# Optimization experiments

Hardware: AMD Instinct MI355X
Metric: run time of the kernel (lower is better)

## Reference

```python
import jax, jax.numpy as jnp
import numpy as np

NUM_HEADS = 16
HEAD_DIM = 64  # latent_dim // num_heads = 1024 // 16


def setup_inputs() -> dict:
    key = jax.random.key(0)
    k1, k2, k3, k4 = jax.random.split(key, 4)
    B, S, C = 4, 2048, 1024
    x = jax.random.normal(k1, (B, S, C), dtype=jnp.float32)
    # torch nn.Linear weight layout: [out_features, in_features]
    W_qkv = jax.random.normal(k2, (2 * 1024 + C, C), dtype=jnp.float32) * (C ** -0.5)
    W_out = jax.random.normal(k3, (C, C), dtype=jnp.float32) * (C ** -0.5)
    b_out = jax.random.normal(k4, (C,), dtype=jnp.float32) * 0.01
    return {"x": x, "W_qkv": W_qkv, "W_out": W_out, "b_out": b_out}


def reference(x, W_qkv, W_out, b_out):
    B, S, C = x.shape
    H, CH = NUM_HEADS, HEAD_DIM
    qkv = jnp.einsum('bsc,oc->bso', x, W_qkv)          # [B, S, 2*latent + C]
    qkv = qkv.reshape(B, S, H, -1)                      # per-head: [CH, CH, C//H]
    q = qkv[..., :CH]
    k = qkv[..., CH:2 * CH]
    v = qkv[..., 2 * CH:]
    energy = jnp.einsum('bqhc,bkhc->bhqk', q, k)        # full score matrix
    scale = jnp.asarray(C, x.dtype) ** 0.5              # note: original scales by sqrt(C), not sqrt(head_dim)
    attn = jax.nn.softmax(energy / scale, axis=-1)
    out = jnp.einsum('bhqk,bkhc->bqhc', attn, v).reshape(B, S, -1)
    out = jnp.einsum('bsc,oc->bso', out, W_out) + b_out
    return out + x
```

## Files before the change

kernel.cpp:

```cpp
#include <hip/hip_runtime.h>
#include <hip/hip_bf16.h>
#include <stdint.h>

#define BB 4
#define SS 2048
#define CC 1024
#define HH 16
#define DD 64
#define MTOT (BB*SS)
#define NQKV 3072

typedef __attribute__((ext_vector_type(8))) short short8;
typedef __attribute__((ext_vector_type(4))) float f32x4;

#define MFMA16(A,B,C) __builtin_amdgcn_mfma_f32_16x16x32_bf16((A),(B),(C),0,0,0)

__device__ __forceinline__ ushort f2bf(float f) {
  uint32_t u = __builtin_bit_cast(uint32_t, f);
  u += 0x7FFFu + ((u >> 16) & 1u);
  return (ushort)(u >> 16);
}

__device__ __forceinline__ unsigned cvtpk(float lo, float hi) {
  unsigned r;
  asm("v_cvt_pk_bf16_f32 %0, %1, %2" : "=v"(r) : "v"(lo), "v"(hi));
  return r;
}

__device__ __forceinline__ float hw_exp2(float x) {
  float r;
  asm("v_exp_f32 %0, %1" : "=v"(r) : "v"(x));
  return r;
}

__global__ void cvt_kernel(const float* __restrict__ src, ushort* __restrict__ dst, int n4) {
  int stride = gridDim.x * blockDim.x;
  for (int i = blockIdx.x * blockDim.x + threadIdx.x; i < n4; i += stride) {
    float4 v = reinterpret_cast<const float4*>(src)[i];
    ushort4 o;
    o.x = f2bf(v.x); o.y = f2bf(v.y); o.z = f2bf(v.z); o.w = f2bf(v.w);
    reinterpret_cast<ushort4*>(dst)[i] = o;
  }
}

__device__ __forceinline__ void stage8k(const ushort* g0, int ldk, ushort* lds, int wave, int lane) {
  #pragma unroll
  for (int r = 0; r < 2; ++r) {
    int chunk = r * 256 + wave * 64 + lane;
    int row = chunk >> 2;
    int co  = (chunk & 3) * 8;
    const ushort* src = g0 + (size_t)row * ldk + co;
    ushort* dst = lds + (size_t)(r * 256 + wave * 64) * 8;
    __builtin_amdgcn_global_load_lds(
        (const __attribute__((address_space(1))) uint32_t*)src,
        (__attribute__((address_space(3))) uint32_t*)dst, 16, 0, 0);
  }
}

__device__ __forceinline__ void gemm_loop(const ushort* __restrict__ A, const ushort* __restrict__ Bw,
                                          int m0, int n0, ushort* As, ushort* Bs, f32x4 acc[4][4]) {
  const int lane = threadIdx.x & 63, wave = threadIdx.x >> 6;
  const int g = lane >> 4, q = lane & 15;
  const int wm = (wave >> 1) * 64, wn = (wave & 1) * 64;
  const ushort* Ag = A + (size_t)m0 * 1024;
  const ushort* Bg = Bw + (size_t)n0 * 1024;
  #pragma unroll 1
  for (int k0 = 0; k0 < 1024; k0 += 32) {
    stage8k(Ag + k0, 1024, As, wave, lane);
    stage8k(Bg + k0, 1024, Bs, wave, lane);
    __syncthreads();
    short8 af[4], bf[4];
    #pragma unroll
    for (int i = 0; i < 4; ++i)
      af[i] = *(const short8*)(As + (wm + i * 16 + q) * 32 + g * 8);
    #pragma unroll
    for (int j = 0; j < 4; ++j)
      bf[j] = *(const short8*)(Bs + (wn + j * 16 + q) * 32 + g * 8);
    #pragma unroll
    for (int i = 0; i < 4; ++i)
      #pragma unroll
      for (int j = 0; j < 4; ++j)
        acc[i][j] = MFMA16(af[i], bf[j], acc[i][j]);
    __syncthreads();
  }
}

__global__ __launch_bounds__(256) void gemm_qkv(const ushort* __restrict__ xb, const ushort* __restrict__ wqkv,
                                                ushort* __restrict__ qfbuf, ushort* __restrict__ kfbuf,
                                                ushort* __restrict__ vfbuf) {
  __shared__ ushort As[128 * 32], Bs[128 * 32];
  const int m0 = blockIdx.x * 128, n0 = blockIdx.y * 128;
  f32x4 acc[4][4];
  #pragma unroll
  for (int i = 0; i < 4; ++i)
    #pragma unroll
    for (int j = 0; j < 4; ++j) acc[i][j] = f32x4{0.f, 0.f, 0.f, 0.f};
  gemm_loop(xb, wqkv, m0, n0, As, Bs, acc);

  const int lane = threadIdx.x & 63, wave = threadIdx.x >> 6;
  const int g = lane >> 4, q = lane & 15;
  const int wm = (wave >> 1) * 64, wn = (wave & 1) * 64;
  #pragma unroll
  for (int j = 0; j < 4; ++j) {
    int n = n0 + wn + j * 16 + q;
    int h = n / 192;
    int rem = n - h * 192;
    int which = rem >> 6;
    int c = rem & 63;
    float scl = (which == 0) ? 0.045084222f : 1.0f;
    #pragma unroll
    for (int i = 0; i < 4; ++i) {
      int mb = m0 + wm + i * 16 + g * 4;
      #pragma unroll
      for (int r = 0; r < 4; ++r) {
        int m = mb + r;
        int b = m >> 11, s = m & 2047;
        int bh = b * 16 + h;
        ushort val = f2bf(acc[i][j][r] * scl);
        if (which < 2) {
          int jt = s >> 4, c0 = c >> 5, lane2 = ((c >> 3) & 3) * 16 + (s & 15), e = c & 7;
          size_t idx = ((((size_t)bh * 128 + jt) * 2 + c0) * 64 + lane2) * 8 + e;
          if (which == 0) qfbuf[idx] = val; else kfbuf[idx] = val;
        } else {
          int jc = s >> 5, gg = (s >> 3) & 3, e = s & 7, ct = c >> 4, qq = c & 15;
          size_t idx = ((((size_t)bh * 64 + jc) * 4 + ct) * 64 + gg * 16 + qq) * 8 + e;
          vfbuf[idx] = val;
        }
      }
    }
  }
}


__device__ __forceinline__ void attn_step(const short8 kf[4][2], const short8 vf[2][4],
                                          const short8 qf[2][2], const short8 onesf,
                                          f32x4 oa[2][4], f32x4 la[2],
                                          ushort* pw0, int g, int q) {
  const f32x4 zed = {0.f, 0.f, 0.f, 0.f};
  #pragma unroll
  for (int t = 0; t < 2; ++t) {
    f32x4 sa[4];
    __builtin_amdgcn_s_setprio(1);
    #pragma unroll
    for (int jt = 0; jt < 4; ++jt) {
      sa[jt] = MFMA16(kf[jt][0], qf[t][0], zed);
      sa[jt] = MFMA16(kf[jt][1], qf[t][1], sa[jt]);
    }
    __builtin_amdgcn_s_setprio(0);
    ushort* pw = pw0 + t * 1152;
    #pragma unroll
    for (int jt = 0; jt < 4; ++jt) {
      uint2 w;
      w.x = cvtpk(hw_exp2(sa[jt][0]), hw_exp2(sa[jt][1]));
      w.y = cvtpk(hw_exp2(sa[jt][2]), hw_exp2(sa[jt][3]));
      *reinterpret_cast<uint2*>(pw + q * 72 + jt * 16 + 4 * g) = w;
    }
    #pragma unroll
    for (int jc = 0; jc < 2; ++jc) {
      short8 pa = *reinterpret_cast<const short8*>(pw + q * 72 + jc * 32 + g * 8);
      __builtin_amdgcn_s_setprio(1);
      #pragma unroll
      for (int ct = 0; ct < 4; ++ct)
        oa[t][ct] = MFMA16(pa, vf[jc][ct], oa[t][ct]);
      la[t] = MFMA16(pa, onesf, la[t]);
      __builtin_amdgcn_s_setprio(0);
    }
  }
}

__global__ __launch_bounds__(256) void attn_kernel(const ushort* __restrict__ QF, const ushort* __restrict__ KF,
                                                   const ushort* __restrict__ VF, ushort* __restrict__ aout) {
  __shared__ ushort Ps[4][2][16 * 72];
  const int bh = blockIdx.x, qb = blockIdx.y;
  const int lane = threadIdx.x & 63, wave = threadIdx.x >> 6;
  const int g = lane >> 4, q = lane & 15;
  const int qt0 = (qb * 4 + wave) * 2;
  const f32x4 zed = {0.f, 0.f, 0.f, 0.f};

  const ushort* Qb = QF + (size_t)bh * 131072 + lane * 8;
  const ushort* Kp = KF + (size_t)bh * 131072 + lane * 8;
  const ushort* Vp = VF + (size_t)bh * 131072 + lane * 8;
  ushort* pw0 = Ps[wave][0];

  short8 onesf;
  #pragma unroll
  for (int e = 0; e < 8; ++e) onesf[e] = (short)0x3F80;

  short8 qf[2][2];
  #pragma unroll
  for (int t = 0; t < 2; ++t)
    #pragma unroll
    for (int c0 = 0; c0 < 2; ++c0)
      qf[t][c0] = *(const short8*)(Qb + ((size_t)(qt0 + t) * 2 + c0) * 512);

  f32x4 oa[2][4], la[2];
  #pragma unroll
  for (int t = 0; t < 2; ++t) {
    la[t] = zed;
    #pragma unroll
    for (int ct = 0; ct < 4; ++ct) oa[t][ct] = zed;
  }

  short8 kfA[4][2], kfB[4][2], vfA[2][4], vfB[2][4];
  #pragma unroll
  for (int jt = 0; jt < 4; ++jt)
    #pragma unroll
    for (int c0 = 0; c0 < 2; ++c0)
      kfA[jt][c0] = *(const short8*)(Kp + ((size_t)jt * 2 + c0) * 512);

  #pragma unroll 1
  for (int i = 0; i < 32; i += 2) {
    #pragma unroll
    for (int jc = 0; jc < 2; ++jc)
      #pragma unroll
      for (int ct = 0; ct < 4; ++ct)
        vfA[jc][ct] = *(const short8*)(Vp + ((size_t)jc * 4 + ct) * 512);
    #pragma unroll
    for (int jt = 0; jt < 4; ++jt)
      #pragma unroll
      for (int c0 = 0; c0 < 2; ++c0)
        kfB[jt][c0] = *(const short8*)(Kp + 4096 + ((size_t)jt * 2 + c0) * 512);

    attn_step(kfA, vfA, qf, onesf, oa, la, pw0, g, q);

    #pragma unroll
    for (int jc = 0; jc < 2; ++jc)
      #pragma unroll
      for (int ct = 0; ct < 4; ++ct)
        vfB[jc][ct] = *(const short8*)(Vp + 4096 + ((size_t)jc * 4 + ct) * 512);
    if (i + 2 < 32) {
      #pragma unroll
      for (int jt = 0; jt < 4; ++jt)
        #pragma unroll
        for (int c0 = 0; c0 < 2; ++c0)
          kfA[jt][c0] = *(const short8*)(Kp + 8192 + ((size_t)jt * 2 + c0) * 512);
    }

    attn_step(kfB, vfB, qf, onesf, oa, la, pw0, g, q);

    Kp += 8192; Vp += 8192;
  }

  const int b = bh >> 4, h = bh & 15;
  #pragma unroll
  for (int t = 0; t < 2; ++t) {
    float inv[4];
    #pragma unroll
    for (int r = 0; r < 4; ++r) inv[r] = 1.0f / la[t][r];
    #pragma unroll
    for (int ct = 0; ct < 4; ++ct) {
      size_t rowb = (size_t)b * SS + (qt0 + t) * 16 + 4 * g;
      int col = h * DD + ct * 16 + q;
      aout[(rowb + 0) * CC + col] = f2bf(oa[t][ct][0] * inv[0]);
      aout[(rowb + 1) * CC + col] = f2bf(oa[t][ct][1] * inv[1]);
      aout[(rowb + 2) * CC + col] = f2bf(oa[t][ct][2] * inv[2]);
      aout[(rowb + 3) * CC + col] = f2bf(oa[t][ct][3] * inv[3]);
    }
  }
}

__global__ __launch_bounds__(256) void gemm_out(const ushort* __restrict__ ab, const ushort* __restrict__ wout,
                                                const float* __restrict__ x, const float* __restrict__ bias,
                                                float* __restrict__ out) {
  __shared__ ushort As[128 * 32], Bs[128 * 32];
  const int m0 = blockIdx.x * 128, n0 = blockIdx.y * 128;
  f32x4 acc[4][4];
  #pragma unroll
  for (int i = 0; i < 4; ++i)
    #pragma unroll
    for (int j = 0; j < 4; ++j) acc[i][j] = f32x4{0.f, 0.f, 0.f, 0.f};
  gemm_loop(ab, wout, m0, n0, As, Bs, acc);

  const int lane = threadIdx.x & 63, wave = threadIdx.x >> 6;
  const int g = lane >> 4, q = lane & 15;
  const int wm = (wave >> 1) * 64, wn = (wave & 1) * 64;
  #pragma unroll
  for (int j = 0; j < 4; ++j) {
    int n = n0 + wn + j * 16 + q;
    float bj = bias[n];
    #pragma unroll
    for (int i = 0; i < 4; ++i) {
      int mb = m0 + wm + i * 16 + g * 4;
      #pragma unroll
      for (int r = 0; r < 4; ++r) {
        size_t m = (size_t)(mb + r);
        out[m * CC + n] = acc[i][j][r] + bj + x[m * CC + n];
      }
    }
  }
}

extern "C" void kernel_launch(void* const* d_in, const int* in_sizes, int n_in,
                              void* d_out, int out_size, void* d_ws, size_t ws_size,
                              hipStream_t stream) {
  const float* x    = (const float*)d_in[0];
  const float* wqkv = (const float*)d_in[1];
  const float* wout = (const float*)d_in[2];
  const float* bias = (const float*)d_in[3];
  float* out = (float*)d_out;

  ushort* xb    = (ushort*)d_ws;
  ushort* wqkvb = xb + (size_t)8 * 1024 * 1024;
  ushort* woutb = wqkvb + (size_t)3 * 1024 * 1024;
  ushort* qfbuf = woutb + (size_t)1024 * 1024;
  ushort* kfbuf = qfbuf + (size_t)8 * 1024 * 1024;
  ushort* vfbuf = kfbuf + (size_t)8 * 1024 * 1024;
  ushort* aout  = vfbuf + (size_t)8 * 1024 * 1024;

  hipLaunchKernelGGL(cvt_kernel, dim3(2048), dim3(256), 0, stream, x, xb, 8 * 1024 * 1024 / 4);
  hipLaunchKernelGGL(cvt_kernel, dim3(1536), dim3(256), 0, stream, wqkv, wqkvb, 3 * 1024 * 1024 / 4);
  hipLaunchKernelGGL(cvt_kernel, dim3(512), dim3(256), 0, stream, wout, woutb, 1024 * 1024 / 4);

  hipLaunchKernelGGL(gemm_qkv, dim3(MTOT / 128, NQKV / 128), dim3(256), 0, stream,
                     xb, wqkvb, qfbuf, kfbuf, vfbuf);
  hipLaunchKernelGGL(attn_kernel, dim3(BB * HH, SS / 128), dim3(256), 0, stream,
                     qfbuf, kfbuf, vfbuf, aout);
  hipLaunchKernelGGL(gemm_out, dim3(MTOT / 128, CC / 128), dim3(256), 0, stream,
                     aout, woutb, x, bias, out);
}
```

Baseline: 222.5 us.

## Replace QKV GEMM with 256x256-tile, 8-wave, double-buffered swizzled-LDS kernel

Swaps the 128x128 single-buffered QKV projection GEMM for a 256x256 tile kernel with 8 waves, a K-step of 64, XOR-swizzled LDS and asynchronous global-to-LDS prefetch two steps ahead. MFMA work is interleaved with fragment loads and barriers, and the block index is remapped for L2 locality. The intent is more data reuse per tile, less global traffic, and hiding load latency behind MFMAs. In exchange it uses a full 128KB of LDS and many accumulator registers, which limits occupancy, and leaves only 384 blocks.

```diff
diff --git a/kernel.cpp b/kernel.cpp
--- a/kernel.cpp
+++ b/kernel.cpp
@@ -33,6 +33,9 @@
   return r;
 }
 
+#define BARRIER() asm volatile("s_barrier" ::: "memory")
+#define LGKM0()   asm volatile("s_waitcnt lgkmcnt(0)" ::: "memory")
+
 __global__ void cvt_kernel(const float* __restrict__ src, ushort* __restrict__ dst, int n4) {
   int stride = gridDim.x * blockDim.x;
   for (int i = blockIdx.x * blockDim.x + threadIdx.x; i < n4; i += stride) {
@@ -40,6 +43,175 @@
     ushort4 o;
     o.x = f2bf(v.x); o.y = f2bf(v.y); o.z = f2bf(v.z); o.w = f2bf(v.w);
     reinterpret_cast<ushort4*>(dst)[i] = o;
+  }
+}
+
+
+__device__ __forceinline__ void stage_half8(const ushort* __restrict__ gsrc, ushort* lds_region, int tid) {
+  #pragma unroll
+  for (int r = 0; r < 2; ++r) {
+    int ci = r * 512 + tid;
+    int row = ci >> 3, slot = ci & 7;
+    const ushort* src = gsrc + (size_t)row * 1024 + ((slot ^ (row & 7)) << 3);
+    ushort* dst = lds_region + ci * 8;
+    __builtin_amdgcn_global_load_lds(
+        (const __attribute__((address_space(1))) uint32_t*)src,
+        (__attribute__((address_space(3))) uint32_t*)dst, 16, 0, 0);
+  }
+}
+
+__device__ __forceinline__ short8 lds_frag(const ushort* L, int region, int R, int slot) {
+  int h = R >> 7, hrow = R & 127;
+  int sl = slot ^ (hrow & 7);
+  return *(const short8*)(L + (region + h) * 8192 + hrow * 64 + sl * 8);
+}
+
+__global__ __launch_bounds__(512, 2) void gemm_qkv8(const ushort* __restrict__ xb, const ushort* __restrict__ wqkv,
+                                                    ushort* __restrict__ qfbuf, ushort* __restrict__ kfbuf,
+                                                    ushort* __restrict__ vfbuf) {
+  __shared__ ushort L[65536];
+  const int tid = threadIdx.x;
+  const int lane = tid & 63;
+  const int q = lane & 15, g = lane >> 4;
+  const int w = tid >> 6, wm = w >> 2, wn = w & 3;
+  const int sw = (blockIdx.x & 7) * 48 + (blockIdx.x >> 3);
+  const int m0 = (sw & 31) * 256, n0 = (sw >> 5) * 256;
+
+  f32x4 acc[8][4];
+  #pragma unroll
+  for (int mi = 0; mi < 8; ++mi)
+    #pragma unroll
+    for (int nj = 0; nj < 4; ++nj) acc[mi][nj] = f32x4{0.f, 0.f, 0.f, 0.f};
+
+  #pragma unroll
+  for (int tt = 0; tt < 2; ++tt) {
+    stage_half8(xb   + (size_t)m0 * 1024        + tt * 64, L + (tt * 4 + 0) * 8192, tid);
+    stage_half8(xb   + (size_t)(m0 + 128) * 1024 + tt * 64, L + (tt * 4 + 1) * 8192, tid);
+    stage_half8(wqkv + (size_t)n0 * 1024        + tt * 64, L + (tt * 4 + 2) * 8192, tid);
+    stage_half8(wqkv + (size_t)(n0 + 128) * 1024 + tt * 64, L + (tt * 4 + 3) * 8192, tid);
+  }
+  asm volatile("s_waitcnt vmcnt(8)" ::: "memory");
+  BARRIER();
+
+  short8 fa[4][2], fb0[2][2], fb1[2][2];
+
+  #pragma unroll 1
+  for (int t = 0; t < 16; ++t) {
+    const int buf = t & 1;
+    const int Ar = buf * 4, Br = buf * 4 + 2;
+    const bool pre = (t + 2 < 16);
+    const int kst = (t + 2) * 64;
+
+    #pragma unroll
+    for (int mi = 0; mi < 4; ++mi)
+      #pragma unroll
+      for (int ks = 0; ks < 2; ++ks)
+        fa[mi][ks] = lds_frag(L, Ar, wm * 128 + mi * 16 + q, ks * 4 + g);
+    #pragma unroll
+    for (int nj = 0; nj < 2; ++nj)
+      #pragma unroll
+      for (int ks = 0; ks < 2; ++ks)
+        fb0[nj][ks] = lds_frag(L, Br, wn * 64 + nj * 16 + q, ks * 4 + g);
+    BARRIER(); LGKM0();
+    __builtin_amdgcn_sched_barrier(0);
+    __builtin_amdgcn_s_setprio(1);
+    #pragma unroll
+    for (int mi = 0; mi < 4; ++mi)
+      #pragma unroll
+      for (int nj = 0; nj < 2; ++nj) {
+        acc[mi][nj] = MFMA16(fa[mi][0], fb0[nj][0], acc[mi][nj]);
+        acc[mi][nj] = MFMA16(fa[mi][1], fb0[nj][1], acc[mi][nj]);
+      }
+    __builtin_amdgcn_s_setprio(0);
+    BARRIER();
+
+    #pragma unroll
+    for (int nj = 0; nj < 2; ++nj)
+      #pragma unroll
+      for (int ks = 0; ks < 2; ++ks)
+        fb1[nj][ks] = lds_frag(L, Br, wn * 64 + (nj + 2) * 16 + q, ks * 4 + g);
+    BARRIER(); LGKM0();
+    __builtin_amdgcn_sched_barrier(0);
+    __builtin_amdgcn_s_setprio(1);
+    #pragma unroll
+    for (int mi = 0; mi < 4; ++mi)
+      #pragma unroll
+      for (int nj = 0; nj < 2; ++nj) {
+        acc[mi][nj + 2] = MFMA16(fa[mi][0], fb1[nj][0], acc[mi][nj + 2]);
+        acc[mi][nj + 2] = MFMA16(fa[mi][1], fb1[nj][1], acc[mi][nj + 2]);
+      }
+    __builtin_amdgcn_s_setprio(0);
+    BARRIER();
+
+    #pragma unroll
+    for (int mi = 0; mi < 4; ++mi)
+      #pragma unroll
+      for (int ks = 0; ks < 2; ++ks)
+        fa[mi][ks] = lds_frag(L, Ar, wm * 128 + (mi + 4) * 16 + q, ks * 4 + g);
+    if (pre) {
+      stage_half8(wqkv + (size_t)n0 * 1024        + kst, L + (Br + 0) * 8192, tid);
+      stage_half8(wqkv + (size_t)(n0 + 128) * 1024 + kst, L + (Br + 1) * 8192, tid);
+    }
+    BARRIER(); LGKM0();
+    __builtin_amdgcn_sched_barrier(0);
+    __builtin_amdgcn_s_setprio(1);
+    #pragma unroll
+    for (int mi = 0; mi < 4; ++mi)
+      #pragma unroll
+      for (int nj = 0; nj < 2; ++nj) {
+        acc[mi + 4][nj + 2] = MFMA16(fa[mi][0], fb1[nj][0], acc[mi + 4][nj + 2]);
+        acc[mi + 4][nj + 2] = MFMA16(fa[mi][1], fb1[nj][1], acc[mi + 4][nj + 2]);
+      }
+    __builtin_amdgcn_s_setprio(0);
+    BARRIER();
+
+    if (pre) {
+      stage_half8(xb + (size_t)m0 * 1024        + kst, L + (Ar + 0) * 8192, tid);
+      stage_half8(xb + (size_t)(m0 + 128) * 1024 + kst, L + (Ar + 1) * 8192, tid);
+    }
+    BARRIER();
+    __builtin_amdgcn_s_setprio(1);
+    #pragma unroll
+    for (int mi = 0; mi < 4; ++mi)
+      #pragma unroll
+      for (int nj = 0; nj < 2; ++nj) {
+        acc[mi + 4][nj] = MFMA16(fa[mi][0], fb0[nj][0], acc[mi + 4][nj]);
+        acc[mi + 4][nj] = MFMA16(fa[mi][1], fb0[nj][1], acc[mi + 4][nj]);
+      }
+    __builtin_amdgcn_s_setprio(0);
+    if (pre) { asm volatile("s_waitcnt vmcnt(8)" ::: "memory"); }
+    else     { asm volatile("s_waitcnt vmcnt(0)" ::: "memory"); }
+    BARRIER();
+  }
+
+  #pragma unroll
+  for (int nj = 0; nj < 4; ++nj) {
+    int n = n0 + wn * 64 + nj * 16 + q;
+    int h = n / 192;
+    int rem = n - h * 192;
+    int which = rem >> 6;
+    int c = rem & 63;
+    float scl = (which == 0) ? 0.045084222f : 1.0f;
+    #pragma unroll
+    for (int mi = 0; mi < 8; ++mi) {
+      int mb = m0 + wm * 128 + mi * 16 + g * 4;
+      #pragma unroll
+      for (int r = 0; r < 4; ++r) {
+        int m = mb + r;
+        int b = m >> 11, s2 = m & 2047;
+        int bh = b * 16 + h;
+        ushort val = f2bf(acc[mi][nj][r] * scl);
+        if (which < 2) {
+          int jt = s2 >> 4, c0 = c >> 5, lane2 = ((c >> 3) & 3) * 16 + (s2 & 15), e = c & 7;
+          size_t idx = ((((size_t)bh * 128 + jt) * 2 + c0) * 64 + lane2) * 8 + e;
+          if (which == 0) qfbuf[idx] = val; else kfbuf[idx] = val;
+        } else {
+          int jc = s2 >> 5, gg = (s2 >> 3) & 3, e = s2 & 7, ct = c >> 4, qq = c & 15;
+          size_t idx = ((((size_t)bh * 64 + jc) * 4 + ct) * 64 + gg * 16 + qq) * 8 + e;
+          vfbuf[idx] = val;
+        }
+      }
+    }
   }
 }
 
@@ -85,53 +257,6 @@
   }
 }
 
-__global__ __launch_bounds__(256) void gemm_qkv(const ushort* __restrict__ xb, const ushort* __restrict__ wqkv,
-                                                ushort* __restrict__ qfbuf, ushort* __restrict__ kfbuf,
-                                                ushort* __restrict__ vfbuf) {
-  __shared__ ushort As[128 * 32], Bs[128 * 32];
-  const int m0 = blockIdx.x * 128, n0 = blockIdx.y * 128;
-  f32x4 acc[4][4];
-  #pragma unroll
-  for (int i = 0; i < 4; ++i)
-    #pragma unroll
-    for (int j = 0; j < 4; ++j) acc[i][j] = f32x4{0.f, 0.f, 0.f, 0.f};
-  gemm_loop(xb, wqkv, m0, n0, As, Bs, acc);
-
-  const int lane = threadIdx.x & 63, wave = threadIdx.x >> 6;
-  const int g = lane >> 4, q = lane & 15;
-  const int wm = (wave >> 1) * 64, wn = (wave & 1) * 64;
-  #pragma unroll
-  for (int j = 0; j < 4; ++j) {
-    int n = n0 + wn + j * 16 + q;
-    int h = n / 192;
-    int rem = n - h * 192;
-    int which = rem >> 6;
-    int c = rem & 63;
-    float scl = (which == 0) ? 0.045084222f : 1.0f;
-    #pragma unroll
-    for (int i = 0; i < 4; ++i) {
-      int mb = m0 + wm + i * 16 + g * 4;
-      #pragma unroll
-      for (int r = 0; r < 4; ++r) {
-        int m = mb + r;
-        int b = m >> 11, s = m & 2047;
-        int bh = b * 16 + h;
-        ushort val = f2bf(acc[i][j][r] * scl);
-        if (which < 2) {
-          int jt = s >> 4, c0 = c >> 5, lane2 = ((c >> 3) & 3) * 16 + (s & 15), e = c & 7;
-          size_t idx = ((((size_t)bh * 128 + jt) * 2 + c0) * 64 + lane2) * 8 + e;
-          if (which == 0) qfbuf[idx] = val; else kfbuf[idx] = val;
-        } else {
-          int jc = s >> 5, gg = (s >> 3) & 3, e = s & 7, ct = c >> 4, qq = c & 15;
-          size_t idx = ((((size_t)bh * 64 + jc) * 4 + ct) * 64 + gg * 16 + qq) * 8 + e;
-          vfbuf[idx] = val;
-        }
-      }
-    }
-  }
-}
-
-
 __device__ __forceinline__ void attn_step(const short8 kf[4][2], const short8 vf[2][4],
                                           const short8 qf[2][2], const short8 onesf,
                                           f32x4 oa[2][4], f32x4 la[2],
@@ -150,10 +275,10 @@
     ushort* pw = pw0 + t * 1152;
     #pragma unroll
     for (int jt = 0; jt < 4; ++jt) {
-      uint2 w;
-      w.x = cvtpk(hw_exp2(sa[jt][0]), hw_exp2(sa[jt][1]));
-      w.y = cvtpk(hw_exp2(sa[jt][2]), hw_exp2(sa[jt][3]));
-      *reinterpret_cast<uint2*>(pw + q * 72 + jt * 16 + 4 * g) = w;
+      uint2 wv;
+      wv.x = cvtpk(hw_exp2(sa[jt][0]), hw_exp2(sa[jt][1]));
+      wv.y = cvtpk(hw_exp2(sa[jt][2]), hw_exp2(sa[jt][3]));
+      *reinterpret_cast<uint2*>(pw + q * 72 + jt * 16 + 4 * g) = wv;
     }
     #pragma unroll
     for (int jc = 0; jc < 2; ++jc) {
@@ -311,7 +436,7 @@
   hipLaunchKernelGGL(cvt_kernel, dim3(1536), dim3(256), 0, stream, wqkv, wqkvb, 3 * 1024 * 1024 / 4);
   hipLaunchKernelGGL(cvt_kernel, dim3(512), dim3(256), 0, stream, wout, woutb, 1024 * 1024 / 4);
 
-  hipLaunchKernelGGL(gemm_qkv, dim3(MTOT / 128, NQKV / 128), dim3(256), 0, stream,
+  hipLaunchKernelGGL(gemm_qkv8, dim3(384), dim3(512), 0, stream,
                      xb, wqkvb, qfbuf, kfbuf, vfbuf);
   hipLaunchKernelGGL(attn_kernel, dim3(BB * HH, SS / 128), dim3(256), 0, stream,
                      qfbuf, kfbuf, vfbuf, aout);
```

Measured after the change: 222.2 us. About the same (-0.1%).

## Double-buffer GEMM mainloop with K=64 tiles, XOR-swizzled LDS, and block swizzle

Applied to the files above, without the earlier changes.

Rewrites the shared GEMM core used by the QKV and output projections. It now stages K=64 slices into two LDS buffers so the next tile's global-to-LDS loads overlap the current tile's MFMAs, using explicit vmcnt waits and raw s_barrier. It also XOR-swizzles the LDS layout to avoid bank conflicts, remaps block IDs for L2 locality, and sets launch bounds to allow two blocks per CU. The cost is 64 KB of LDS per block, which may limit occupancy, and hand-written waitcnt/barrier logic that must match the number of outstanding loads.

```diff
diff --git a/kernel.cpp b/kernel.cpp
--- a/kernel.cpp
+++ b/kernel.cpp
@@ -14,6 +14,7 @@
 typedef __attribute__((ext_vector_type(4))) float f32x4;
 
 #define MFMA16(A,B,C) __builtin_amdgcn_mfma_f32_16x16x32_bf16((A),(B),(C),0,0,0)
+#define BARRIER() asm volatile("s_barrier" ::: "memory")
 
 __device__ __forceinline__ ushort f2bf(float f) {
   uint32_t u = __builtin_bit_cast(uint32_t, f);
@@ -43,59 +44,89 @@
   }
 }
 
-__device__ __forceinline__ void stage8k(const ushort* g0, int ldk, ushort* lds, int wave, int lane) {
-  #pragma unroll
-  for (int r = 0; r < 2; ++r) {
-    int chunk = r * 256 + wave * 64 + lane;
-    int row = chunk >> 2;
-    int co  = (chunk & 3) * 8;
-    const ushort* src = g0 + (size_t)row * ldk + co;
-    ushort* dst = lds + (size_t)(r * 256 + wave * 64) * 8;
+
+__device__ __forceinline__ void stage_half128(const ushort* __restrict__ gsrc, ushort* ldsbase, int tid) {
+  #pragma unroll
+  for (int ld = 0; ld < 4; ++ld) {
+    int ci = ld * 256 + tid;
+    int row = ci >> 3, slot = ci & 7;
+    const ushort* src = gsrc + (size_t)row * 1024 + ((slot ^ (row & 7)) << 3);
     __builtin_amdgcn_global_load_lds(
         (const __attribute__((address_space(1))) uint32_t*)src,
-        (__attribute__((address_space(3))) uint32_t*)dst, 16, 0, 0);
-  }
-}
-
-__device__ __forceinline__ void gemm_loop(const ushort* __restrict__ A, const ushort* __restrict__ Bw,
-                                          int m0, int n0, ushort* As, ushort* Bs, f32x4 acc[4][4]) {
-  const int lane = threadIdx.x & 63, wave = threadIdx.x >> 6;
-  const int g = lane >> 4, q = lane & 15;
-  const int wm = (wave >> 1) * 64, wn = (wave & 1) * 64;
+        (__attribute__((address_space(3))) uint32_t*)(ldsbase + ci * 8), 16, 0, 0);
+  }
+}
+
+__device__ __forceinline__ short8 rd_frag(const ushort* Lb, int row, int slot) {
+  return *(const short8*)(Lb + row * 64 + ((slot ^ (row & 7)) << 3));
+}
+
+__device__ __forceinline__ void core128(const ushort* __restrict__ A, const ushort* __restrict__ Bw,
+                                        int m0, int n0, ushort* L, f32x4 acc[4][4]) {
+  const int tid = threadIdx.x, lane = tid & 63, w = tid >> 6;
+  const int q = lane & 15, g = lane >> 4;
+  const int wm = (w >> 1) * 64, wn = (w & 1) * 64;
   const ushort* Ag = A + (size_t)m0 * 1024;
   const ushort* Bg = Bw + (size_t)n0 * 1024;
+
+  #pragma unroll
+  for (int tt = 0; tt < 2; ++tt) {
+    stage_half128(Ag + tt * 64, L + tt * 16384, tid);
+    stage_half128(Bg + tt * 64, L + tt * 16384 + 8192, tid);
+  }
+  asm volatile("s_waitcnt vmcnt(8)" ::: "memory");
+  BARRIER();
+
   #pragma unroll 1
-  for (int k0 = 0; k0 < 1024; k0 += 32) {
-    stage8k(Ag + k0, 1024, As, wave, lane);
-    stage8k(Bg + k0, 1024, Bs, wave, lane);
-    __syncthreads();
-    short8 af[4], bf[4];
-    #pragma unroll
-    for (int i = 0; i < 4; ++i)
-      af[i] = *(const short8*)(As + (wm + i * 16 + q) * 32 + g * 8);
-    #pragma unroll
-    for (int j = 0; j < 4; ++j)
-      bf[j] = *(const short8*)(Bs + (wn + j * 16 + q) * 32 + g * 8);
-    #pragma unroll
-    for (int i = 0; i < 4; ++i)
-      #pragma unroll
-      for (int j = 0; j < 4; ++j)
-        acc[i][j] = MFMA16(af[i], bf[j], acc[i][j]);
-    __syncthreads();
-  }
-}
-
-__global__ __launch_bounds__(256) void gemm_qkv(const ushort* __restrict__ xb, const ushort* __restrict__ wqkv,
-                                                ushort* __restrict__ qfbuf, ushort* __restrict__ kfbuf,
-                                                ushort* __restrict__ vfbuf) {
-  __shared__ ushort As[128 * 32], Bs[128 * 32];
-  const int m0 = blockIdx.x * 128, n0 = blockIdx.y * 128;
+  for (int t = 0; t < 16; ++t) {
+    const ushort* La = L + (t & 1) * 16384;
+    const ushort* Lb = La + 8192;
+    short8 af[4][2], bf[4][2];
+    #pragma unroll
+    for (int mi = 0; mi < 4; ++mi)
+      #pragma unroll
+      for (int ks = 0; ks < 2; ++ks)
+        af[mi][ks] = rd_frag(La, wm + mi * 16 + q, ks * 4 + g);
+    #pragma unroll
+    for (int nj = 0; nj < 4; ++nj)
+      #pragma unroll
+      for (int ks = 0; ks < 2; ++ks)
+        bf[nj][ks] = rd_frag(Lb, wn + nj * 16 + q, ks * 4 + g);
+    #pragma unroll
+    for (int mi = 0; mi < 4; ++mi)
+      #pragma unroll
+      for (int nj = 0; nj < 4; ++nj) {
+        acc[mi][nj] = MFMA16(af[mi][0], bf[nj][0], acc[mi][nj]);
+        acc[mi][nj] = MFMA16(af[mi][1], bf[nj][1], acc[mi][nj]);
+      }
+    BARRIER();
+    if (t <= 13) {
+      ushort* Ls = L + (t & 1) * 16384;
+      stage_half128(Ag + (t + 2) * 64, Ls, tid);
+      stage_half128(Bg + (t + 2) * 64, Ls + 8192, tid);
+      asm volatile("s_waitcnt vmcnt(8)" ::: "memory");
+      BARRIER();
+    } else if (t == 14) {
+      asm volatile("s_waitcnt vmcnt(0)" ::: "memory");
+      BARRIER();
+    }
+  }
+}
+
+__global__ __launch_bounds__(256, 2) void gemm_qkv(const ushort* __restrict__ xb, const ushort* __restrict__ wqkv,
+                                                   ushort* __restrict__ qfbuf, ushort* __restrict__ kfbuf,
+                                                   ushort* __restrict__ vfbuf) {
+  __shared__ __align__(16) ushort L[32768];
+  const int bid = blockIdx.x;
+  const int sw = (bid & 7) * 192 + (bid >> 3);
+  const int m0 = (sw & 63) * 128, n0 = (sw >> 6) * 128;
+
   f32x4 acc[4][4];
   #pragma unroll
   for (int i = 0; i < 4; ++i)
     #pragma unroll
     for (int j = 0; j < 4; ++j) acc[i][j] = f32x4{0.f, 0.f, 0.f, 0.f};
-  gemm_loop(xb, wqkv, m0, n0, As, Bs, acc);
+  core128(xb, wqkv, m0, n0, L, acc);
 
   const int lane = threadIdx.x & 63, wave = threadIdx.x >> 6;
   const int g = lane >> 4, q = lane & 15;
@@ -131,6 +162,39 @@
   }
 }
 
+__global__ __launch_bounds__(256, 2) void gemm_out(const ushort* __restrict__ ab, const ushort* __restrict__ wout,
+                                                   const float* __restrict__ x, const float* __restrict__ bias,
+                                                   float* __restrict__ out) {
+  __shared__ __align__(16) ushort L[32768];
+  const int bid = blockIdx.x;
+  const int sw = (bid & 7) * 64 + (bid >> 3);
+  const int m0 = (sw & 63) * 128, n0 = (sw >> 6) * 128;
+
+  f32x4 acc[4][4];
+  #pragma unroll
+  for (int i = 0; i < 4; ++i)
+    #pragma unroll
+    for (int j = 0; j < 4; ++j) acc[i][j] = f32x4{0.f, 0.f, 0.f, 0.f};
+  core128(ab, wout, m0, n0, L, acc);
+
+  const int lane = threadIdx.x & 63, wave = threadIdx.x >> 6;
+  const int g = lane >> 4, q = lane & 15;
+  const int wm = (wave >> 1) * 64, wn = (wave & 1) * 64;
+  #pragma unroll
+  for (int j = 0; j < 4; ++j) {
+    int n = n0 + wn + j * 16 + q;
+    float bj = bias[n];
+    #pragma unroll
+    for (int i = 0; i < 4; ++i) {
+      int mb = m0 + wm + i * 16 + g * 4;
+      #pragma unroll
+      for (int r = 0; r < 4; ++r) {
+        size_t m = (size_t)(mb + r);
+        out[m * CC + n] = acc[i][j][r] + bj + x[m * CC + n];
+      }
+    }
+  }
+}
 
 __device__ __forceinline__ void attn_step(const short8 kf[4][2], const short8 vf[2][4],
                                           const short8 qf[2][2], const short8 onesf,
@@ -150,10 +214,10 @@
     ushort* pw = pw0 + t * 1152;
     #pragma unroll
     for (int jt = 0; jt < 4; ++jt) {
-      uint2 w;
-      w.x = cvtpk(hw_exp2(sa[jt][0]), hw_exp2(sa[jt][1]));
-      w.y = cvtpk(hw_exp2(sa[jt][2]), hw_exp2(sa[jt][3]));
-      *reinterpret_cast<uint2*>(pw + q * 72 + jt * 16 + 4 * g) = w;
+      uint2 wv;
+      wv.x = cvtpk(hw_exp2(sa[jt][0]), hw_exp2(sa[jt][1]));
+      wv.y = cvtpk(hw_exp2(sa[jt][2]), hw_exp2(sa[jt][3]));
+      *reinterpret_cast<uint2*>(pw + q * 72 + jt * 16 + 4 * g) = wv;
     }
     #pragma unroll
     for (int jc = 0; jc < 2; ++jc) {
@@ -259,37 +323,6 @@
   }
 }
 
-__global__ __launch_bounds__(256) void gemm_out(const ushort* __restrict__ ab, const ushort* __restrict__ wout,
-                                                const float* __restrict__ x, const float* __restrict__ bias,
-                                                float* __restrict__ out) {
-  __shared__ ushort As[128 * 32], Bs[128 * 32];
-  const int m0 = blockIdx.x * 128, n0 = blockIdx.y * 128;
-  f32x4 acc[4][4];
-  #pragma unroll
-  for (int i = 0; i < 4; ++i)
-    #pragma unroll
-    for (int j = 0; j < 4; ++j) acc[i][j] = f32x4{0.f, 0.f, 0.f, 0.f};
-  gemm_loop(ab, wout, m0, n0, As, Bs, acc);
-
-  const int lane = threadIdx.x & 63, wave = threadIdx.x >> 6;
-  const int g = lane >> 4, q = lane & 15;
-  const int wm = (wave >> 1) * 64, wn = (wave & 1) * 64;
-  #pragma unroll
-  for (int j = 0; j < 4; ++j) {
-    int n = n0 + wn + j * 16 + q;
-    float bj = bias[n];
-    #pragma unroll
-    for (int i = 0; i < 4; ++i) {
-      int mb = m0 + wm + i * 16 + g * 4;
-      #pragma unroll
-      for (int r = 0; r < 4; ++r) {
-        size_t m = (size_t)(mb + r);
-        out[m * CC + n] = acc[i][j][r] + bj + x[m * CC + n];
-      }
-    }
-  }
-}
-
 extern "C" void kernel_launch(void* const* d_in, const int* in_sizes, int n_in,
                               void* d_out, int out_size, void* d_ws, size_t ws_size,
                               hipStream_t stream) {
@@ -311,10 +344,10 @@
   hipLaunchKernelGGL(cvt_kernel, dim3(1536), dim3(256), 0, stream, wqkv, wqkvb, 3 * 1024 * 1024 / 4);
   hipLaunchKernelGGL(cvt_kernel, dim3(512), dim3(256), 0, stream, wout, woutb, 1024 * 1024 / 4);
 
-  hipLaunchKernelGGL(gemm_qkv, dim3(MTOT / 128, NQKV / 128), dim3(256), 0, stream,
+  hipLaunchKernelGGL(gemm_qkv, dim3(1536), dim3(256), 0, stream,
                      xb, wqkvb, qfbuf, kfbuf, vfbuf);
   hipLaunchKernelGGL(attn_kernel, dim3(BB * HH, SS / 128), dim3(256), 0, stream,
                      qfbuf, kfbuf, vfbuf, aout);
-  hipLaunchKernelGGL(gemm_out, dim3(MTOT / 128, CC / 128), dim3(256), 0, stream,
+  hipLaunchKernelGGL(gemm_out, dim3(512), dim3(256), 0, stream,
                      aout, woutb, x, bias, out);
 }
```

Result: faster. 211.2 us (-5.1%).
